# Performance work log

Measured on AMD Instinct MI355X. Metric: run time of the kernel, lower is better.

Reference implementation:

```python
import jax, jax.numpy as jnp
import numpy as np

# GraphVToS (keras) faithful jax reference.
# Original math: for every atom pair (i,j), concat(vf[i], vf[j]) along features,
# project with w_vs [2F,K] + b_vs, multiply by pairwise distance vector d[i,j,c],
# sum over coordinate axis c (=3), apply activation.
# We avoid materializing the [B,N,N,3,2F] tile by splitting w_vs into the halves
# acting on vf[i] and vf[j] (exact same linear map, distributivity of concat-matmul).

B, N, C, F, K = 8, 128, 3, 64, 64

def setup_inputs() -> dict:
    key = jax.random.key(0)
    k1, k2, k3 = jax.random.split(key, 3)
    vector_features = jax.random.normal(k1, (B, N, C, F), dtype=jnp.float32)
    distances = jax.random.normal(k2, (B, N, N, C), dtype=jnp.float32)
    w_vs = jax.random.normal(k3, (2 * F, K), dtype=jnp.float32) * (1.0 / np.sqrt(2 * F))
    b_vs = jnp.zeros((K,), dtype=jnp.float32)
    return {"vector_features": vector_features, "distances": distances,
            "w_vs": w_vs, "b_vs": b_vs}

def reference(vector_features, distances, w_vs, b_vs):
    f = vector_features.shape[-1]
    w_i, w_j = w_vs[:f], w_vs[f:]          # halves acting on vf[i] / vf[j]
    # Per-atom projections: [B,N,C,K]
    p_i = jnp.einsum('bncf,fk->bnck', vector_features, w_i)
    p_j = jnp.einsum('bncf,fk->bnck', vector_features, w_j)
    # Distance-weighted reduction over coordinate axis c -> [B,N,N,K]
    s = (jnp.einsum('bick,bijc->bijk', p_i, distances)
         + jnp.einsum('bjck,bijc->bijk', p_j, distances))
    # Bias contributes b_vs * sum_c d[i,j,c]
    s = s + distances.sum(axis=-1)[..., None] * b_vs
    return jax.nn.relu(s)
```

## Files before the change

### kernel.cpp

```cpp
#include <hip/hip_runtime.h>

#define Bz 8
#define Nz 128
#define Cz 3
#define Fz 64
#define Kz 64

typedef float v4f __attribute__((ext_vector_type(4)));

__global__ __launch_bounds__(256) void proj_kernel(const float* __restrict__ vf,
                                                   const float4* __restrict__ w4,
                                                   const float4* __restrict__ bv4,
                                                   float4* __restrict__ P4) {
    int idx = blockIdx.x * blockDim.x + threadIdx.x;
    const int PER4 = (Bz * Nz * Cz * Kz) / 4;
    int which = idx / PER4;
    int rem   = idx - which * PER4;
    int k4 = rem & 15;
    int c  = (rem >> 4) % Cz;
    int bn = rem / (Cz * Kz / 4);

    const float*  vrow = vf + (bn * Cz + c) * Fz;
    const float4* wcol = w4 + which * (Fz * Kz / 4) + k4;

    float4 acc = make_float4(0.f, 0.f, 0.f, 0.f);
    #pragma unroll 8
    for (int f = 0; f < Fz; ++f) {
        float v = vrow[f];
        float4 wv = wcol[f * 16];
        acc.x += v * wv.x; acc.y += v * wv.y; acc.z += v * wv.z; acc.w += v * wv.w;
    }
    if (which == 0) {
        float4 bv = bv4[k4];
        acc.x += bv.x; acc.y += bv.y; acc.z += bv.z; acc.w += bv.w;
    }
    P4[idx] = acc;
}

__global__ __launch_bounds__(256) void pair_kernel(const float* __restrict__ d,
                                                   const v4f* __restrict__ P4,
                                                   v4f* __restrict__ out4) {
    const int PER4 = (Bz * Nz * Cz * Kz) / 4;
    __shared__ float ds[64 * Cz];

    int t  = threadIdx.x;
    int bi = blockIdx.x >> 1;
    int jh = blockIdx.x & 1;
    int i  = bi & (Nz - 1);
    int b  = bi >> 7;

    const float* drow = d + ((b * Nz + i) * Nz + jh * 64) * Cz;
    if (t < 48) {
        ((v4f*)ds)[t] = __builtin_nontemporal_load((const v4f*)drow + t);
    }

    int k4 = t & 15;
    int jg = (t >> 4) & 15;

    const v4f* pi = P4 + (b * Nz + i) * 48 + k4;
    v4f a0 = pi[0], a1 = pi[16], a2 = pi[32];

    __syncthreads();

    const v4f* pjb = P4 + PER4 + (b * Nz + jh * 64) * 48 + k4;
    v4f*       ob  = out4 + ((b * Nz + i) * Nz + jh * 64) * 16 + k4;

    #pragma unroll
    for (int jj = 0; jj < 4; ++jj) {
        int jl = jg * 4 + jj;
        float d0 = ds[jl * 3 + 0], d1 = ds[jl * 3 + 1], d2 = ds[jl * 3 + 2];

        const v4f* pj = pjb + jl * 48;
        v4f c0 = pj[0], c1 = pj[16], c2 = pj[32];

        v4f r = d0 * (a0 + c0) + d1 * (a1 + c1) + d2 * (a2 + c2);
        r.x = fmaxf(r.x, 0.f);
        r.y = fmaxf(r.y, 0.f);
        r.z = fmaxf(r.z, 0.f);
        r.w = fmaxf(r.w, 0.f);
        __builtin_nontemporal_store(r, ob + jl * 16);
    }
}

extern "C" void kernel_launch(void* const* d_in, const int* in_sizes, int n_in,
                              void* d_out, int out_size, void* d_ws, size_t ws_size,
                              hipStream_t stream) {
    const float* vf  = (const float*)d_in[0];
    const float* dst = (const float*)d_in[1];
    const float* w   = (const float*)d_in[2];
    const float* bvs = (const float*)d_in[3];
    float* out = (float*)d_out;
    float* P   = (float*)d_ws;

    proj_kernel<<<384, 256, 0, stream>>>(vf, (const float4*)w,
                                         (const float4*)bvs, (float4*)P);
    pair_kernel<<<Bz * Nz * 2, 256, 0, stream>>>(dst, (const v4f*)P, (v4f*)out);
}
```

Baseline: 80.53 us.

## Process two i rows per pair block and stage vf rows in shared memory

```diff
diff --git a/kernel.cpp b/kernel.cpp
--- a/kernel.cpp
+++ b/kernel.cpp
@@ -8,77 +8,83 @@
 
 typedef float v4f __attribute__((ext_vector_type(4)));
 
-__global__ __launch_bounds__(256) void proj_kernel(const float* __restrict__ vf,
-                                                   const float4* __restrict__ w4,
-                                                   const float4* __restrict__ bv4,
-                                                   float4* __restrict__ P4) {
-    int idx = blockIdx.x * blockDim.x + threadIdx.x;
-    const int PER4 = (Bz * Nz * Cz * Kz) / 4;
-    int which = idx / PER4;
-    int rem   = idx - which * PER4;
-    int k4 = rem & 15;
-    int c  = (rem >> 4) % Cz;
-    int bn = rem / (Cz * Kz / 4);
+__global__ __launch_bounds__(256) void proj_kernel(const v4f* __restrict__ vf4,
+                                                   const v4f* __restrict__ w4,
+                                                   const v4f* __restrict__ bv4,
+                                                   v4f* __restrict__ P4) {
+    __shared__ float vs[16 * 72];
+    int t = threadIdx.x;
+    int which = (blockIdx.x >= 192) ? 1 : 0;
+    int rem_base = (blockIdx.x - which * 192) * 256;
+    int bnc_base = rem_base >> 4;
 
-    const float*  vrow = vf + (bn * Cz + c) * Fz;
-    const float4* wcol = w4 + which * (Fz * Kz / 4) + k4;
+    int lr = t >> 4;
+    int ls = t & 15;
+    *(v4f*)&vs[lr * 72 + ls * 4] = vf4[bnc_base * 16 + t];
+    __syncthreads();
 
-    float4 acc = make_float4(0.f, 0.f, 0.f, 0.f);
+    int k4 = t & 15;
+    const v4f* wcol = w4 + which * (Fz * Kz / 4) + k4;
+
+    v4f acc = {0.f, 0.f, 0.f, 0.f};
     #pragma unroll 8
     for (int f = 0; f < Fz; ++f) {
-        float v = vrow[f];
-        float4 wv = wcol[f * 16];
-        acc.x += v * wv.x; acc.y += v * wv.y; acc.z += v * wv.z; acc.w += v * wv.w;
+        float v = vs[lr * 72 + f];
+        acc += v * wcol[f * 16];
     }
-    if (which == 0) {
-        float4 bv = bv4[k4];
-        acc.x += bv.x; acc.y += bv.y; acc.z += bv.z; acc.w += bv.w;
-    }
-    P4[idx] = acc;
+    if (which == 0) acc += bv4[k4];
+    P4[which * 49152 + rem_base + t] = acc;
 }
 
 __global__ __launch_bounds__(256) void pair_kernel(const float* __restrict__ d,
                                                    const v4f* __restrict__ P4,
                                                    v4f* __restrict__ out4) {
     const int PER4 = (Bz * Nz * Cz * Kz) / 4;
-    __shared__ float ds[64 * Cz];
+    __shared__ float ds[2 * 192];
 
     int t  = threadIdx.x;
-    int bi = blockIdx.x >> 1;
     int jh = blockIdx.x & 1;
-    int i  = bi & (Nz - 1);
-    int b  = bi >> 7;
+    int ip = (blockIdx.x >> 1) & 63;
+    int b  = blockIdx.x >> 7;
+    int i0 = ip * 2;
 
-    const float* drow = d + ((b * Nz + i) * Nz + jh * 64) * Cz;
-    if (t < 48) {
-        ((v4f*)ds)[t] = __builtin_nontemporal_load((const v4f*)drow + t);
+    if (t < 96) {
+        int ir = (t >= 48) ? 1 : 0;
+        int cc = t - ir * 48;
+        const float* drow = d + ((b * Nz + i0 + ir) * Nz + jh * 64) * Cz;
+        ((v4f*)ds)[ir * 48 + cc] = __builtin_nontemporal_load((const v4f*)drow + cc);
     }
 
     int k4 = t & 15;
     int jg = (t >> 4) & 15;
 
-    const v4f* pi = P4 + (b * Nz + i) * 48 + k4;
-    v4f a0 = pi[0], a1 = pi[16], a2 = pi[32];
+    const v4f* pi = P4 + (b * Nz + i0) * 48 + k4;
+    v4f a00 = pi[0],  a01 = pi[16], a02 = pi[32];
+    v4f a10 = pi[48], a11 = pi[64], a12 = pi[80];
 
     __syncthreads();
 
     const v4f* pjb = P4 + PER4 + (b * Nz + jh * 64) * 48 + k4;
-    v4f*       ob  = out4 + ((b * Nz + i) * Nz + jh * 64) * 16 + k4;
+    v4f* ob0 = out4 + ((b * Nz + i0) * Nz + jh * 64) * 16 + k4;
+    v4f* ob1 = ob0 + Nz * 16;
 
     #pragma unroll
     for (int jj = 0; jj < 4; ++jj) {
         int jl = jg * 4 + jj;
-        float d0 = ds[jl * 3 + 0], d1 = ds[jl * 3 + 1], d2 = ds[jl * 3 + 2];
-
         const v4f* pj = pjb + jl * 48;
         v4f c0 = pj[0], c1 = pj[16], c2 = pj[32];
 
-        v4f r = d0 * (a0 + c0) + d1 * (a1 + c1) + d2 * (a2 + c2);
-        r.x = fmaxf(r.x, 0.f);
-        r.y = fmaxf(r.y, 0.f);
-        r.z = fmaxf(r.z, 0.f);
-        r.w = fmaxf(r.w, 0.f);
-        __builtin_nontemporal_store(r, ob + jl * 16);
+        float d00 = ds[jl * 3], d01 = ds[jl * 3 + 1], d02 = ds[jl * 3 + 2];
+        float d10 = ds[192 + jl * 3], d11 = ds[192 + jl * 3 + 1], d12 = ds[192 + jl * 3 + 2];
+
+        v4f r0 = d00 * (a00 + c0) + d01 * (a01 + c1) + d02 * (a02 + c2);
+        v4f r1 = d10 * (a10 + c0) + d11 * (a11 + c1) + d12 * (a12 + c2);
+        r0.x = fmaxf(r0.x, 0.f); r0.y = fmaxf(r0.y, 0.f);
+        r0.z = fmaxf(r0.z, 0.f); r0.w = fmaxf(r0.w, 0.f);
+        r1.x = fmaxf(r1.x, 0.f); r1.y = fmaxf(r1.y, 0.f);
+        r1.z = fmaxf(r1.z, 0.f); r1.w = fmaxf(r1.w, 0.f);
+        ob0[jl * 16] = r0;
+        ob1[jl * 16] = r1;
     }
 }
 
@@ -92,7 +98,7 @@
     float* out = (float*)d_out;
     float* P   = (float*)d_ws;
 
-    proj_kernel<<<384, 256, 0, stream>>>(vf, (const float4*)w,
-                                         (const float4*)bvs, (float4*)P);
-    pair_kernel<<<Bz * Nz * 2, 256, 0, stream>>>(dst, (const v4f*)P, (v4f*)out);
+    proj_kernel<<<384, 256, 0, stream>>>((const v4f*)vf, (const v4f*)w,
+                                         (const v4f*)bvs, (v4f*)P);
+    pair_kernel<<<Bz * (Nz / 2) * 2, 256, 0, stream>>>(dst, (const v4f*)P, (v4f*)out);
 }
```

Result: faster. 78.46 us (-2.6%).
